# Kernel tuning notes

Hardware: AMD Instinct MI355X
Metric: run time of the kernel (lower is better)

## Reference

```python
import jax, jax.numpy as jnp
import numpy as np

N_NODES = 100000   # adj is [N, N], x is [N, D]
N_EDGES = 625000   # nnz of the COO adjacency
D_FEAT = 128       # embedding dim
EDGE_DROPOUT = 0.1


def setup_inputs() -> dict:
    key = jax.random.key(0)
    k1, k2, k3, k4 = jax.random.split(key, 4)
    x = jax.random.normal(k1, (N_NODES, D_FEAT), dtype=jnp.float32)
    edge_vals = jax.random.uniform(k2, (N_EDGES,), dtype=jnp.float32)
    edge_index = jax.random.randint(k3, (2, N_EDGES), 0, N_NODES)
    # training-mode edge dropout mask: keep edge iff u > edge_dropout
    keep_mask = jax.random.uniform(k4, (N_EDGES,)) > EDGE_DROPOUT
    return {"x": x, "edge_vals": edge_vals, "edge_index": edge_index, "keep_mask": keep_mask}


def reference(x, edge_vals, edge_index, keep_mask):
    # Dropping an edge from the COO tensor == zeroing its value in the SpMM.
    vals = jnp.where(keep_mask, edge_vals, jnp.zeros((), dtype=edge_vals.dtype))
    row = edge_index[0]  # destination rows of adj
    col = edge_index[1]  # source columns of adj
    # out[r] = sum_{e: row[e]==r} vals[e] * x[col[e]]   (torch.sparse.mm(adj, x))
    msgs = vals[:, None] * x[col]                      # [E, D]
    return jax.ops.segment_sum(msgs, row, num_segments=N_NODES)
```

## Files before the change

kernel.cpp:

```cpp
#include <hip/hip_runtime.h>

#define N_NODES 100000
#define N_EDGES 625000
#define D_FEAT  128

#define BKT_SHIFT 10
#define BKT_ROWS  1024
#define NBKT      ((N_NODES + BKT_ROWS - 1) / BKT_ROWS)
#define EPB       2048
#define ABLOCKS   ((N_EDGES + EPB - 1) / EPB)
#define CHCAP     48
#define CAPB      8192
#define CONV_BLOCKS (N_NODES * D_FEAT / 8 / 256)

#define BF_LO(u) __uint_as_float((u) << 16)
#define BF_HI(u) __uint_as_float((u) & 0xffff0000u)

__device__ __forceinline__ unsigned int rne_bf16(unsigned int u) {
    return (u + 0x7fffu + ((u >> 16) & 1u)) >> 16;
}

__global__ __launch_bounds__(256) void scatter_edges(
    const int* __restrict__ ei, const int* __restrict__ keep,
    const float* __restrict__ vals,
    int*  __restrict__ counts,
    int2* __restrict__ chunks)
{
    __shared__ int cur[NBKT];
    int b = blockIdx.x;
    int t = threadIdx.x;
    if (t < NBKT) cur[t] = 0;
    __syncthreads();
    int base = b * EPB;
    int kp[8], rows[8], cols[8]; float vv[8];
    #pragma unroll
    for (int j = 0; j < 2; ++j) {
        int eb = base + j * 1024 + t * 4;
        if (eb + 4 <= N_EDGES) {
            int4   k4 = *reinterpret_cast<const int4*>(keep + eb);
            int4   r4 = *reinterpret_cast<const int4*>(ei + eb);
            int4   c4 = *reinterpret_cast<const int4*>(ei + N_EDGES + eb);
            float4 v4 = *reinterpret_cast<const float4*>(vals + eb);
            kp[j*4+0]=k4.x; kp[j*4+1]=k4.y; kp[j*4+2]=k4.z; kp[j*4+3]=k4.w;
            rows[j*4+0]=r4.x; rows[j*4+1]=r4.y; rows[j*4+2]=r4.z; rows[j*4+3]=r4.w;
            cols[j*4+0]=c4.x; cols[j*4+1]=c4.y; cols[j*4+2]=c4.z; cols[j*4+3]=c4.w;
            vv[j*4+0]=v4.x; vv[j*4+1]=v4.y; vv[j*4+2]=v4.z; vv[j*4+3]=v4.w;
        } else {
            #pragma unroll
            for (int q = 0; q < 4; ++q) {
                int e = eb + q;
                bool in = (e < N_EDGES);
                kp[j*4+q]   = in ? keep[e] : 0;
                rows[j*4+q] = in ? ei[e] : 0;
                cols[j*4+q] = in ? ei[N_EDGES + e] : 0;
                vv[j*4+q]   = in ? vals[e] : 0.f;
            }
        }
    }
    #pragma unroll
    for (int j = 0; j < 8; ++j) {
        if (kp[j]) {
            int bk = rows[j] >> BKT_SHIFT;
            int pos = atomicAdd(&cur[bk], 1);
            if (pos < CHCAP) {
                int2 pr = { cols[j] | ((rows[j] & (BKT_ROWS - 1)) << 17),
                            __float_as_int(vv[j]) };
                chunks[((long long)b * NBKT + bk) * CHCAP + pos] = pr;
            }
        }
    }
    __syncthreads();
    if (t < NBKT) counts[b * NBKT + t] = min(cur[t], CHCAP);
}

__global__ __launch_bounds__(256) void csr_conv(
    const float* __restrict__ x, uint4* __restrict__ xb4,
    const int* __restrict__ counts, const int2* __restrict__ chunks,
    int2* __restrict__ fin, int2* __restrict__ rowinfo)
{
    int blk = blockIdx.x;
    if (blk >= NBKT) {
        int i = (blk - NBKT) * 256 + threadIdx.x;
        const float4* x4 = reinterpret_cast<const float4*>(x);
        float4 v0 = x4[i * 2], v1 = x4[i * 2 + 1];
        unsigned int a  = rne_bf16(__float_as_uint(v0.x));
        unsigned int bb = rne_bf16(__float_as_uint(v0.y));
        unsigned int c  = rne_bf16(__float_as_uint(v0.z));
        unsigned int d  = rne_bf16(__float_as_uint(v0.w));
        unsigned int e2 = rne_bf16(__float_as_uint(v1.x));
        unsigned int f  = rne_bf16(__float_as_uint(v1.y));
        unsigned int g  = rne_bf16(__float_as_uint(v1.z));
        unsigned int h  = rne_bf16(__float_as_uint(v1.w));
        uint4 o = { a | (bb << 16), c | (d << 16), e2 | (f << 16), g | (h << 16) };
        xb4[i] = o;
        return;
    }
    __shared__ int2 ebuf[CAPB];
    __shared__ int  cbase[ABLOCKS + 1];
    __shared__ int  hist[BKT_ROWS];
    __shared__ int  ssum[256];
    int b = blk, t = threadIdx.x;

    int i0 = 2 * t, i1 = 2 * t + 1;
    int c0 = (i0 < ABLOCKS) ? counts[i0 * NBKT + b] : 0;
    int c1 = (i1 < ABLOCKS) ? counts[i1 * NBKT + b] : 0;
    ssum[t] = c0 + c1;
    __syncthreads();
    for (int off = 1; off < 256; off <<= 1) {
        int add = (t >= off) ? ssum[t - off] : 0;
        __syncthreads();
        ssum[t] += add;
        __syncthreads();
    }
    int excl = (t == 0) ? 0 : ssum[t - 1];
    if (i0 < ABLOCKS) cbase[i0] = excl;
    if (i1 < ABLOCKS) cbase[i1] = excl + c0;
    if (t == 255) cbase[ABLOCKS] = ssum[255];
    __syncthreads();
    int ntot = cbase[ABLOCKS]; if (ntot > CAPB) ntot = CAPB;

    for (int c = t; c < ABLOCKS; c += 256) {
        int n  = counts[c * NBKT + b];
        int cb = cbase[c];
        const int2* src = chunks + ((long long)c * NBKT + b) * CHCAP;
        for (int k = 0; k < n; ++k) {
            int dst = cb + k;
            if (dst < CAPB) ebuf[dst] = src[k];
        }
    }
    for (int i = t; i < BKT_ROWS; i += 256) hist[i] = 0;
    __syncthreads();

    for (int i = t; i < ntot; i += 256)
        atomicAdd(&hist[(ebuf[i].x >> 17) & (BKT_ROWS - 1)], 1);
    __syncthreads();

    int t4 = t * 4;
    int h0 = hist[t4], h1 = hist[t4 + 1], h2 = hist[t4 + 2], h3 = hist[t4 + 3];
    ssum[t] = h0 + h1 + h2 + h3;
    __syncthreads();
    for (int off = 1; off < 256; off <<= 1) {
        int add = (t >= off) ? ssum[t - off] : 0;
        __syncthreads();
        ssum[t] += add;
        __syncthreads();
    }
    int ex = (t == 0) ? 0 : ssum[t - 1];
    int s0 = ex, s1 = ex + h0, s2 = ex + h0 + h1, s3 = ex + h0 + h1 + h2;
    hist[t4] = s0; hist[t4 + 1] = s1; hist[t4 + 2] = s2; hist[t4 + 3] = s3;

    int rbase = b << BKT_SHIFT;
    int gbase = b * CAPB;
    int st[4] = { s0, s1, s2, s3 };
    int hh[4] = { h0, h1, h2, h3 };
    #pragma unroll
    for (int i = 0; i < 4; ++i) {
        int row = rbase + t4 + i;
        if (row < N_NODES) {
            int2 ri = { gbase + st[i], hh[i] };
            rowinfo[row] = ri;
        }
    }
    __syncthreads();

    for (int i = t; i < ntot; i += 256) {
        int2 pr = ebuf[i];
        int rl = (pr.x >> 17) & (BKT_ROWS - 1);
        int pos = atomicAdd(&hist[rl], 1);
        if (pos < CAPB) {
            int2 o = { pr.x & 0x1FFFF, pr.y };
            fin[gbase + pos] = o;
        }
    }
}

__global__ __launch_bounds__(256) void csr_only(
    const int* __restrict__ counts, const int2* __restrict__ chunks,
    int2* __restrict__ fin, int2* __restrict__ rowinfo)
{
    __shared__ int2 ebuf[CAPB];
    __shared__ int  cbase[ABLOCKS + 1];
    __shared__ int  hist[BKT_ROWS];
    __shared__ int  ssum[256];
    int b = blockIdx.x, t = threadIdx.x;
    int i0 = 2 * t, i1 = 2 * t + 1;
    int c0 = (i0 < ABLOCKS) ? counts[i0 * NBKT + b] : 0;
    int c1 = (i1 < ABLOCKS) ? counts[i1 * NBKT + b] : 0;
    ssum[t] = c0 + c1;
    __syncthreads();
    for (int off = 1; off < 256; off <<= 1) {
        int add = (t >= off) ? ssum[t - off] : 0;
        __syncthreads();
        ssum[t] += add;
        __syncthreads();
    }
    int excl = (t == 0) ? 0 : ssum[t - 1];
    if (i0 < ABLOCKS) cbase[i0] = excl;
    if (i1 < ABLOCKS) cbase[i1] = excl + c0;
    if (t == 255) cbase[ABLOCKS] = ssum[255];
    __syncthreads();
    int ntot = cbase[ABLOCKS]; if (ntot > CAPB) ntot = CAPB;
    for (int c = t; c < ABLOCKS; c += 256) {
        int n  = counts[c * NBKT + b];
        int cb = cbase[c];
        const int2* src = chunks + ((long long)c * NBKT + b) * CHCAP;
        for (int k = 0; k < n; ++k) {
            int dst = cb + k;
            if (dst < CAPB) ebuf[dst] = src[k];
        }
    }
    for (int i = t; i < BKT_ROWS; i += 256) hist[i] = 0;
    __syncthreads();
    for (int i = t; i < ntot; i += 256)
        atomicAdd(&hist[(ebuf[i].x >> 17) & (BKT_ROWS - 1)], 1);
    __syncthreads();
    int t4 = t * 4;
    int h0 = hist[t4], h1 = hist[t4 + 1], h2 = hist[t4 + 2], h3 = hist[t4 + 3];
    ssum[t] = h0 + h1 + h2 + h3;
    __syncthreads();
    for (int off = 1; off < 256; off <<= 1) {
        int add = (t >= off) ? ssum[t - off] : 0;
        __syncthreads();
        ssum[t] += add;
        __syncthreads();
    }
    int ex = (t == 0) ? 0 : ssum[t - 1];
    int s0 = ex, s1 = ex + h0, s2 = ex + h0 + h1, s3 = ex + h0 + h1 + h2;
    hist[t4] = s0; hist[t4 + 1] = s1; hist[t4 + 2] = s2; hist[t4 + 3] = s3;
    int rbase = b << BKT_SHIFT;
    int gbase = b * CAPB;
    int st[4] = { s0, s1, s2, s3 };
    int hh[4] = { h0, h1, h2, h3 };
    #pragma unroll
    for (int i = 0; i < 4; ++i) {
        int row = rbase + t4 + i;
        if (row < N_NODES) {
            int2 ri = { gbase + st[i], hh[i] };
            rowinfo[row] = ri;
        }
    }
    __syncthreads();
    for (int i = t; i < ntot; i += 256) {
        int2 pr = ebuf[i];
        int rl = (pr.x >> 17) & (BKT_ROWS - 1);
        int pos = atomicAdd(&hist[rl], 1);
        if (pos < CAPB) {
            int2 o = { pr.x & 0x1FFFF, pr.y };
            fin[gbase + pos] = o;
        }
    }
}

__global__ __launch_bounds__(256) void gather_csr_bf16(
    const uint4* __restrict__ xb4, const int2* __restrict__ rowinfo,
    const int2* __restrict__ fin, float4* __restrict__ out4)
{
    int gid = blockIdx.x * blockDim.x + threadIdx.x;
    int wave = gid >> 6;
    int lane = threadIdx.x & 63;
    int sub = lane >> 4, l16 = lane & 15;
    int row = wave * 4 + sub;
    if (row >= N_NODES) return;
    int2 ri = rowinfo[row];
    const int2* bp = fin + ri.x;
    int n = ri.y;

    float a0=0,a1=0,a2=0,a3=0,a4=0,a5=0,a6=0,a7=0;
    float c0=0,c1=0,c2=0,c3=0,c4=0,c5=0,c6=0,c7=0;
    int p = 0;
    for (; p + 4 <= n; p += 4) {
        int2 e0 = bp[p], e1 = bp[p + 1], e2 = bp[p + 2], e3 = bp[p + 3];
        uint4 g0 = xb4[(long long)e0.x * 16 + l16];
        uint4 g1 = xb4[(long long)e1.x * 16 + l16];
        uint4 g2 = xb4[(long long)e2.x * 16 + l16];
        uint4 g3 = xb4[(long long)e3.x * 16 + l16];
        float v0 = __int_as_float(e0.y), v1 = __int_as_float(e1.y);
        float v2 = __int_as_float(e2.y), v3 = __int_as_float(e3.y);
        a0 += v0 * BF_LO(g0.x); a1 += v0 * BF_HI(g0.x);
        a2 += v0 * BF_LO(g0.y); a3 += v0 * BF_HI(g0.y);
        a4 += v0 * BF_LO(g0.z); a5 += v0 * BF_HI(g0.z);
        a6 += v0 * BF_LO(g0.w); a7 += v0 * BF_HI(g0.w);
        c0 += v1 * BF_LO(g1.x); c1 += v1 * BF_HI(g1.x);
        c2 += v1 * BF_LO(g1.y); c3 += v1 * BF_HI(g1.y);
        c4 += v1 * BF_LO(g1.z); c5 += v1 * BF_HI(g1.z);
        c6 += v1 * BF_LO(g1.w); c7 += v1 * BF_HI(g1.w);
        a0 += v2 * BF_LO(g2.x); a1 += v2 * BF_HI(g2.x);
        a2 += v2 * BF_LO(g2.y); a3 += v2 * BF_HI(g2.y);
        a4 += v2 * BF_LO(g2.z); a5 += v2 * BF_HI(g2.z);
        a6 += v2 * BF_LO(g2.w); a7 += v2 * BF_HI(g2.w);
        c0 += v3 * BF_LO(g3.x); c1 += v3 * BF_HI(g3.x);
        c2 += v3 * BF_LO(g3.y); c3 += v3 * BF_HI(g3.y);
        c4 += v3 * BF_LO(g3.z); c5 += v3 * BF_HI(g3.z);
        c6 += v3 * BF_LO(g3.w); c7 += v3 * BF_HI(g3.w);
    }
    if (p + 2 <= n) {
        int2 e0 = bp[p], e1 = bp[p + 1];
        uint4 g0 = xb4[(long long)e0.x * 16 + l16];
        uint4 g1 = xb4[(long long)e1.x * 16 + l16];
        float v0 = __int_as_float(e0.y), v1 = __int_as_float(e1.y);
        a0 += v0 * BF_LO(g0.x); a1 += v0 * BF_HI(g0.x);
        a2 += v0 * BF_LO(g0.y); a3 += v0 * BF_HI(g0.y);
        a4 += v0 * BF_LO(g0.z); a5 += v0 * BF_HI(g0.z);
        a6 += v0 * BF_LO(g0.w); a7 += v0 * BF_HI(g0.w);
        c0 += v1 * BF_LO(g1.x); c1 += v1 * BF_HI(g1.x);
        c2 += v1 * BF_LO(g1.y); c3 += v1 * BF_HI(g1.y);
        c4 += v1 * BF_LO(g1.z); c5 += v1 * BF_HI(g1.z);
        c6 += v1 * BF_LO(g1.w); c7 += v1 * BF_HI(g1.w);
        p += 2;
    }
    if (p < n) {
        int2 e = bp[p];
        uint4 g = xb4[(long long)e.x * 16 + l16];
        float v = __int_as_float(e.y);
        a0 += v * BF_LO(g.x); a1 += v * BF_HI(g.x);
        a2 += v * BF_LO(g.y); a3 += v * BF_HI(g.y);
        a4 += v * BF_LO(g.z); a5 += v * BF_HI(g.z);
        a6 += v * BF_LO(g.w); a7 += v * BF_HI(g.w);
    }
    float4 o0 = { a0 + c0, a1 + c1, a2 + c2, a3 + c3 };
    float4 o1 = { a4 + c4, a5 + c5, a6 + c6, a7 + c7 };
    long long ob = (long long)row * 32 + l16 * 2;
    out4[ob]     = o0;
    out4[ob + 1] = o1;
}

__global__ __launch_bounds__(256) void gather_csr_f32(
    const float* __restrict__ x, const int2* __restrict__ rowinfo,
    const int2* __restrict__ fin, float* __restrict__ out)
{
    int gid = blockIdx.x * blockDim.x + threadIdx.x;
    int row = gid >> 6;
    if (row >= N_NODES) return;
    int lane = threadIdx.x & 63;
    int2 ri = rowinfo[row];
    const int2* bp = fin + ri.x;
    int n = ri.y;
    int d = lane * 2;
    float a0 = 0.f, b0 = 0.f, a1 = 0.f, b1 = 0.f;
    int p = 0;
    for (; p + 2 <= n; p += 2) {
        int2 e0 = bp[p], e1 = bp[p + 1];
        float2 x0 = *reinterpret_cast<const float2*>(x + (long long)e0.x * D_FEAT + d);
        float2 x1 = *reinterpret_cast<const float2*>(x + (long long)e1.x * D_FEAT + d);
        float v0 = __int_as_float(e0.y), v1 = __int_as_float(e1.y);
        a0 += v0 * x0.x; b0 += v0 * x0.y;
        a1 += v1 * x1.x; b1 += v1 * x1.y;
    }
    if (p < n) {
        int2 e = bp[p];
        float2 xv = *reinterpret_cast<const float2*>(x + (long long)e.x * D_FEAT + d);
        float v = __int_as_float(e.y);
        a0 += v * xv.x; b0 += v * xv.y;
    }
    float2 o = { a0 + a1, b0 + b1 };
    *reinterpret_cast<float2*>(out + (long long)row * D_FEAT + d) = o;
}

static inline size_t alignup(size_t v) { return (v + 511) / 512 * 512; }

extern "C" void kernel_launch(void* const* d_in, const int* in_sizes, int n_in,
                              void* d_out, int out_size, void* d_ws, size_t ws_size,
                              hipStream_t stream) {
    const float* x    = (const float*)d_in[0];
    const float* vals = (const float*)d_in[1];
    const int*   ei   = (const int*)d_in[2];
    const int*   keep = (const int*)d_in[3];
    float* out = (float*)d_out;

    const size_t sz_xb     = alignup((size_t)N_NODES * D_FEAT * 2);
    const size_t sz_counts = alignup((size_t)ABLOCKS * NBKT * 4);
    const size_t sz_chunks = alignup((size_t)ABLOCKS * NBKT * CHCAP * 8);
    const size_t sz_fin    = alignup((size_t)NBKT * CAPB * 8);
    const size_t sz_ri     = alignup((size_t)N_NODES * 8);
    const bool use_bf16 =
        ws_size >= sz_xb + sz_counts + sz_chunks + sz_fin + sz_ri;

    char* ws = (char*)d_ws;
    uint4* xb4 = nullptr;
    if (use_bf16) { xb4 = (uint4*)ws; ws += sz_xb; }
    int*  counts  = (int*)ws;   ws += sz_counts;
    int2* chunks  = (int2*)ws;  ws += sz_chunks;
    int2* fin     = (int2*)ws;  ws += sz_fin;
    int2* rowinfo = (int2*)ws;

    scatter_edges<<<ABLOCKS, 256, 0, stream>>>(ei, keep, vals, counts, chunks);

    if (use_bf16) {
        csr_conv<<<NBKT + CONV_BLOCKS, 256, 0, stream>>>(
            x, xb4, counts, chunks, fin, rowinfo);
        const long long gthreads = (long long)((N_NODES + 3) / 4) * 64;
        gather_csr_bf16<<<(int)((gthreads + 255) / 256), 256, 0, stream>>>(
            xb4, rowinfo, fin, (float4*)out);
    } else {
        csr_only<<<NBKT, 256, 0, stream>>>(counts, chunks, fin, rowinfo);
        const long long gthreads = (long long)N_NODES * 64;
        gather_csr_f32<<<(int)((gthreads + 255) / 256), 256, 0, stream>>>(
            x, rowinfo, fin, out);
    }
}
```

Measured before the change: 65.93 us.

## Sort rows by degree within each bucket to balance gather waves

The CSR build kernel now takes a per-bucket histogram of row degrees (capped at 63), runs a wave-level prefix scan over it, and writes a permutation array that orders each bucket's rows by degree. The bf16 gather kernel reads its row through this permutation, so the four rows sharing a wave have similar edge counts. This is meant to cut the idle lanes and loop divergence caused by mixing rows of different lengths in one wave. It costs an extra workspace array, a few shared-memory atomics and barriers in the CSR build, one more dependent load per row in the gather, and less locality in output writes.

```diff
diff --git a/kernel.cpp b/kernel.cpp
--- a/kernel.cpp
+++ b/kernel.cpp
@@ -76,7 +76,8 @@
 __global__ __launch_bounds__(256) void csr_conv(
     const float* __restrict__ x, uint4* __restrict__ xb4,
     const int* __restrict__ counts, const int2* __restrict__ chunks,
-    int2* __restrict__ fin, int2* __restrict__ rowinfo)
+    int2* __restrict__ fin, int2* __restrict__ rowinfo,
+    int* __restrict__ order)
 {
     int blk = blockIdx.x;
     if (blk >= NBKT) {
@@ -99,6 +100,7 @@
     __shared__ int  cbase[ABLOCKS + 1];
     __shared__ int  hist[BKT_ROWS];
     __shared__ int  ssum[256];
+    __shared__ int  dh[64];
     int b = blk, t = threadIdx.x;
 
     int i0 = 2 * t, i1 = 2 * t + 1;
@@ -172,95 +174,49 @@
             fin[gbase + pos] = o;
         }
     }
-}
-
-__global__ __launch_bounds__(256) void csr_only(
-    const int* __restrict__ counts, const int2* __restrict__ chunks,
-    int2* __restrict__ fin, int2* __restrict__ rowinfo)
-{
-    __shared__ int2 ebuf[CAPB];
-    __shared__ int  cbase[ABLOCKS + 1];
-    __shared__ int  hist[BKT_ROWS];
-    __shared__ int  ssum[256];
-    int b = blockIdx.x, t = threadIdx.x;
-    int i0 = 2 * t, i1 = 2 * t + 1;
-    int c0 = (i0 < ABLOCKS) ? counts[i0 * NBKT + b] : 0;
-    int c1 = (i1 < ABLOCKS) ? counts[i1 * NBKT + b] : 0;
-    ssum[t] = c0 + c1;
-    __syncthreads();
-    for (int off = 1; off < 256; off <<= 1) {
-        int add = (t >= off) ? ssum[t - off] : 0;
-        __syncthreads();
-        ssum[t] += add;
-        __syncthreads();
-    }
-    int excl = (t == 0) ? 0 : ssum[t - 1];
-    if (i0 < ABLOCKS) cbase[i0] = excl;
-    if (i1 < ABLOCKS) cbase[i1] = excl + c0;
-    if (t == 255) cbase[ABLOCKS] = ssum[255];
-    __syncthreads();
-    int ntot = cbase[ABLOCKS]; if (ntot > CAPB) ntot = CAPB;
-    for (int c = t; c < ABLOCKS; c += 256) {
-        int n  = counts[c * NBKT + b];
-        int cb = cbase[c];
-        const int2* src = chunks + ((long long)c * NBKT + b) * CHCAP;
-        for (int k = 0; k < n; ++k) {
-            int dst = cb + k;
-            if (dst < CAPB) ebuf[dst] = src[k];
-        }
-    }
-    for (int i = t; i < BKT_ROWS; i += 256) hist[i] = 0;
-    __syncthreads();
-    for (int i = t; i < ntot; i += 256)
-        atomicAdd(&hist[(ebuf[i].x >> 17) & (BKT_ROWS - 1)], 1);
-    __syncthreads();
-    int t4 = t * 4;
-    int h0 = hist[t4], h1 = hist[t4 + 1], h2 = hist[t4 + 2], h3 = hist[t4 + 3];
-    ssum[t] = h0 + h1 + h2 + h3;
-    __syncthreads();
-    for (int off = 1; off < 256; off <<= 1) {
-        int add = (t >= off) ? ssum[t - off] : 0;
-        __syncthreads();
-        ssum[t] += add;
-        __syncthreads();
-    }
-    int ex = (t == 0) ? 0 : ssum[t - 1];
-    int s0 = ex, s1 = ex + h0, s2 = ex + h0 + h1, s3 = ex + h0 + h1 + h2;
-    hist[t4] = s0; hist[t4 + 1] = s1; hist[t4 + 2] = s2; hist[t4 + 3] = s3;
-    int rbase = b << BKT_SHIFT;
-    int gbase = b * CAPB;
-    int st[4] = { s0, s1, s2, s3 };
-    int hh[4] = { h0, h1, h2, h3 };
+
+    __syncthreads();
+    if (t < 64) dh[t] = 0;
+    __syncthreads();
+    #pragma unroll
+    for (int i = 0; i < 4; ++i) {
+        int row = rbase + t4 + i;
+        if (row < N_NODES) atomicAdd(&dh[min(hh[i], 63)], 1);
+    }
+    __syncthreads();
+    if (t < 64) {
+        int orig = dh[t];
+        int v = orig;
+        #pragma unroll
+        for (int o = 1; o < 64; o <<= 1) {
+            int u = __shfl_up(v, o, 64);
+            if (t >= o) v += u;
+        }
+        dh[t] = v - orig;
+    }
+    __syncthreads();
     #pragma unroll
     for (int i = 0; i < 4; ++i) {
         int row = rbase + t4 + i;
         if (row < N_NODES) {
-            int2 ri = { gbase + st[i], hh[i] };
-            rowinfo[row] = ri;
-        }
-    }
-    __syncthreads();
-    for (int i = t; i < ntot; i += 256) {
-        int2 pr = ebuf[i];
-        int rl = (pr.x >> 17) & (BKT_ROWS - 1);
-        int pos = atomicAdd(&hist[rl], 1);
-        if (pos < CAPB) {
-            int2 o = { pr.x & 0x1FFFF, pr.y };
-            fin[gbase + pos] = o;
+            int pos = atomicAdd(&dh[min(hh[i], 63)], 1);
+            order[(b << BKT_SHIFT) + pos] = row;
         }
     }
 }
 
 __global__ __launch_bounds__(256) void gather_csr_bf16(
     const uint4* __restrict__ xb4, const int2* __restrict__ rowinfo,
-    const int2* __restrict__ fin, float4* __restrict__ out4)
+    const int2* __restrict__ fin, const int* __restrict__ order,
+    float4* __restrict__ out4)
 {
     int gid = blockIdx.x * blockDim.x + threadIdx.x;
     int wave = gid >> 6;
     int lane = threadIdx.x & 63;
     int sub = lane >> 4, l16 = lane & 15;
-    int row = wave * 4 + sub;
-    if (row >= N_NODES) return;
+    int slot = wave * 4 + sub;
+    if (slot >= N_NODES) return;
+    int row = order[slot];
     int2 ri = rowinfo[row];
     const int2* bp = fin + ri.x;
     int n = ri.y;
@@ -324,6 +280,83 @@
     out4[ob + 1] = o1;
 }
 
+__global__ __launch_bounds__(256) void csr_only(
+    const int* __restrict__ counts, const int2* __restrict__ chunks,
+    int2* __restrict__ fin, int2* __restrict__ rowinfo)
+{
+    __shared__ int2 ebuf[CAPB];
+    __shared__ int  cbase[ABLOCKS + 1];
+    __shared__ int  hist[BKT_ROWS];
+    __shared__ int  ssum[256];
+    int b = blockIdx.x, t = threadIdx.x;
+    int i0 = 2 * t, i1 = 2 * t + 1;
+    int c0 = (i0 < ABLOCKS) ? counts[i0 * NBKT + b] : 0;
+    int c1 = (i1 < ABLOCKS) ? counts[i1 * NBKT + b] : 0;
+    ssum[t] = c0 + c1;
+    __syncthreads();
+    for (int off = 1; off < 256; off <<= 1) {
+        int add = (t >= off) ? ssum[t - off] : 0;
+        __syncthreads();
+        ssum[t] += add;
+        __syncthreads();
+    }
+    int excl = (t == 0) ? 0 : ssum[t - 1];
+    if (i0 < ABLOCKS) cbase[i0] = excl;
+    if (i1 < ABLOCKS) cbase[i1] = excl + c0;
+    if (t == 255) cbase[ABLOCKS] = ssum[255];
+    __syncthreads();
+    int ntot = cbase[ABLOCKS]; if (ntot > CAPB) ntot = CAPB;
+    for (int c = t; c < ABLOCKS; c += 256) {
+        int n  = counts[c * NBKT + b];
+        int cb = cbase[c];
+        const int2* src = chunks + ((long long)c * NBKT + b) * CHCAP;
+        for (int k = 0; k < n; ++k) {
+            int dst = cb + k;
+            if (dst < CAPB) ebuf[dst] = src[k];
+        }
+    }
+    for (int i = t; i < BKT_ROWS; i += 256) hist[i] = 0;
+    __syncthreads();
+    for (int i = t; i < ntot; i += 256)
+        atomicAdd(&hist[(ebuf[i].x >> 17) & (BKT_ROWS - 1)], 1);
+    __syncthreads();
+    int t4 = t * 4;
+    int h0 = hist[t4], h1 = hist[t4 + 1], h2 = hist[t4 + 2], h3 = hist[t4 + 3];
+    ssum[t] = h0 + h1 + h2 + h3;
+    __syncthreads();
+    for (int off = 1; off < 256; off <<= 1) {
+        int add = (t >= off) ? ssum[t - off] : 0;
+        __syncthreads();
+        ssum[t] += add;
+        __syncthreads();
+    }
+    int ex = (t == 0) ? 0 : ssum[t - 1];
+    int s0 = ex, s1 = ex + h0, s2 = ex + h0 + h1, s3 = ex + h0 + h1 + h2;
+    hist[t4] = s0; hist[t4 + 1] = s1; hist[t4 + 2] = s2; hist[t4 + 3] = s3;
+    int rbase = b << BKT_SHIFT;
+    int gbase = b * CAPB;
+    int st[4] = { s0, s1, s2, s3 };
+    int hh[4] = { h0, h1, h2, h3 };
+    #pragma unroll
+    for (int i = 0; i < 4; ++i) {
+        int row = rbase + t4 + i;
+        if (row < N_NODES) {
+            int2 ri = { gbase + st[i], hh[i] };
+            rowinfo[row] = ri;
+        }
+    }
+    __syncthreads();
+    for (int i = t; i < ntot; i += 256) {
+        int2 pr = ebuf[i];
+        int rl = (pr.x >> 17) & (BKT_ROWS - 1);
+        int pos = atomicAdd(&hist[rl], 1);
+        if (pos < CAPB) {
+            int2 o = { pr.x & 0x1FFFF, pr.y };
+            fin[gbase + pos] = o;
+        }
+    }
+}
+
 __global__ __launch_bounds__(256) void gather_csr_f32(
     const float* __restrict__ x, const int2* __restrict__ rowinfo,
     const int2* __restrict__ fin, float* __restrict__ out)
@@ -372,8 +405,9 @@
     const size_t sz_chunks = alignup((size_t)ABLOCKS * NBKT * CHCAP * 8);
     const size_t sz_fin    = alignup((size_t)NBKT * CAPB * 8);
     const size_t sz_ri     = alignup((size_t)N_NODES * 8);
+    const size_t sz_order  = alignup((size_t)NBKT * BKT_ROWS * 4);
     const bool use_bf16 =
-        ws_size >= sz_xb + sz_counts + sz_chunks + sz_fin + sz_ri;
+        ws_size >= sz_xb + sz_counts + sz_chunks + sz_fin + sz_ri + sz_order;
 
     char* ws = (char*)d_ws;
     uint4* xb4 = nullptr;
@@ -381,16 +415,17 @@
     int*  counts  = (int*)ws;   ws += sz_counts;
     int2* chunks  = (int2*)ws;  ws += sz_chunks;
     int2* fin     = (int2*)ws;  ws += sz_fin;
-    int2* rowinfo = (int2*)ws;
+    int2* rowinfo = (int2*)ws;  ws += sz_ri;
+    int*  order   = (int*)ws;
 
     scatter_edges<<<ABLOCKS, 256, 0, stream>>>(ei, keep, vals, counts, chunks);
 
     if (use_bf16) {
         csr_conv<<<NBKT + CONV_BLOCKS, 256, 0, stream>>>(
-            x, xb4, counts, chunks, fin, rowinfo);
+            x, xb4, counts, chunks, fin, rowinfo, order);
         const long long gthreads = (long long)((N_NODES + 3) / 4) * 64;
         gather_csr_bf16<<<(int)((gthreads + 255) / 256), 256, 0, stream>>>(
-            xb4, rowinfo, fin, (float4*)out);
+            xb4, rowinfo, fin, order, (float4*)out);
     } else {
         csr_only<<<NBKT, 256, 0, stream>>>(counts, chunks, fin, rowinfo);
         const long long gthreads = (long long)N_NODES * 64;
```

Result: slower. 68.48 us (+3.9%).
